# Kernel optimization log

Measured on AMD Instinct MI355X. Metric: run time of the kernel, lower is better.

The kernel has to match this reference:

```python
import jax, jax.numpy as jnp
import numpy as np

B, C, H, W = 4, 128, 64, 64


def setup_inputs() -> dict:
    key = jax.random.key(0)
    ks = jax.random.split(key, 10)
    s = 1.0 / np.sqrt(C)  # conv2d default-ish init scale
    return {
        "key_img": jax.random.normal(ks[0], (B, C, H, W), jnp.float32),
        "query_img": jax.random.normal(ks[1], (B, C, H, W), jnp.float32),
        "value_img": jax.random.normal(ks[2], (B, C, H, W), jnp.float32),
        "Wq": jax.random.normal(ks[3], (C, C), jnp.float32) * s,
        "bq": jax.random.normal(ks[4], (C,), jnp.float32) * s,
        "Wk": jax.random.normal(ks[5], (C, C), jnp.float32) * s,
        "bk": jax.random.normal(ks[6], (C,), jnp.float32) * s,
        "Wv": jax.random.normal(ks[7], (C, C), jnp.float32) * s,
        "bv": jax.random.normal(ks[8], (C,), jnp.float32) * s,
        "gamma": jax.random.normal(ks[9], (1,), jnp.float32) * 0.02,
        "tau": jnp.array([0.01], jnp.float32),  # registered buffer
    }


def _conv1x1(x, Wm, b):
    # 1x1 conv == per-pixel channel mixing
    return jnp.einsum("oc,bchw->bohw", Wm, x) + b[None, :, None, None]


def reference(key_img, query_img, value_img, Wq, bq, Wk, bk, Wv, bv, gamma, tau):
    Bv, Cv, Hv, Wd = key_img.shape
    HW = Hv * Wd
    # proj_query: [B, HW, C], channel-mean-subtracted and L2-normalized per pixel
    pq = _conv1x1(query_img, Wq, bq).reshape(Bv, Cv, HW).transpose(0, 2, 1)
    pq = pq - jnp.mean(pq, axis=2, keepdims=True)
    pq = pq / jnp.linalg.norm(pq, axis=2, keepdims=True)
    # proj_key: [B, C, HW], same normalization along channel axis
    pk = _conv1x1(key_img, Wk, bk).reshape(Bv, Cv, HW)
    pk = pk - jnp.mean(pk, axis=1, keepdims=True)
    pk = pk / jnp.linalg.norm(pk, axis=1, keepdims=True)
    # corr_map: [B, HW, HW] (cosine-similarity-like scores)
    corr_map = jnp.einsum("bnc,bcm->bnm", pq, pk)
    conf_map = jnp.max(corr_map, axis=2).reshape(Bv, 1, Hv, Wd)
    attention = jax.nn.softmax(corr_map / tau[0], axis=-1)
    pv = _conv1x1(value_img, Wv, bv).reshape(Bv, Cv, HW)
    # out = proj_value @ attention^T : [B, C, HW]
    out = jnp.einsum("bcm,bnm->bcn", pv, attention).reshape(Bv, Cv, Hv, Wd)
    out = gamma[0] * out + value_img
    return corr_map, conf_map, out
```

## Files before the change

kernel.cpp:

```cpp
#include <hip/hip_runtime.h>
#include <cstdint>
#include <cstddef>

#define B_   4
#define C_   128
#define HW_  4096

typedef _Float16 h16;
typedef _Float16 h16x8 __attribute__((ext_vector_type(8)));
typedef float f32x4v __attribute__((ext_vector_type(4)));
typedef float f32x16v __attribute__((ext_vector_type(16)));

static __device__ __forceinline__ uint32_t cvtpk(float x, float y) {
  auto h = __builtin_amdgcn_cvt_pkrtz(x, y);
  return __builtin_bit_cast(uint32_t, h);
}

static __device__ __forceinline__ void gload_lds16(const void* g, void* l) {
  __builtin_amdgcn_global_load_lds((const __attribute__((address_space(1))) uint32_t*)g,
                                   (__attribute__((address_space(3))) uint32_t*)l, 16, 0, 0);
}

__global__ __launch_bounds__(256) void proj_kernel(
    const float* __restrict__ qimg, const float* __restrict__ kimg, const float* __restrict__ vimg,
    const float* __restrict__ Wq, const float* __restrict__ bq,
    const float* __restrict__ Wk, const float* __restrict__ bk,
    const float* __restrict__ Wv, const float* __restrict__ bv,
    h16* __restrict__ pq, h16* __restrict__ pk, h16* __restrict__ pv)
{
  __shared__ __align__(16) float sm[9216];
  float* wch = sm;
  float* xs  = sm + 4224;
  float* ps  = sm;

  const int tid   = threadIdx.x;
  const int which = blockIdx.y;
  const int p0g   = blockIdx.x * 64;
  const int b     = p0g >> 12;
  const int p0    = p0g & (HW_ - 1);

  const float* x; const float* W; const float* bias;
  if      (which == 0) { x = qimg; W = Wq; bias = bq; }
  else if (which == 1) { x = kimg; W = Wk; bias = bk; }
  else                 { x = vimg; W = Wv; bias = bv; }
  const float* xb = x + (size_t)b * C_ * HW_ + p0;

  const int ogrp = tid >> 3;
  const int pgrp = tid & 7;
  const int obase = ogrp * 4, pbase = pgrp * 8;

  float acc[4][8];
  #pragma unroll
  for (int i = 0; i < 4; ++i) {
    const float bi = bias[obase + i];
    #pragma unroll
    for (int j = 0; j < 8; ++j) acc[i][j] = bi;
  }

  for (int s = 0; s < 4; ++s) {
    #pragma unroll
    for (int it = 0; it < 16; ++it) {
      const int idx = tid + it * 256;
      const int o = idx >> 5, kc = idx & 31;
      wch[o * 33 + kc] = W[o * 128 + s * 32 + kc];
    }
    #pragma unroll
    for (int it = 0; it < 8; ++it) {
      const int idx = tid + it * 256;
      const int c = idx >> 6, p = idx & 63;
      xs[c * 72 + p] = xb[(size_t)(s * 32 + c) * HW_ + p];
    }
    __syncthreads();
    #pragma unroll 4
    for (int k = 0; k < 32; ++k) {
      const float4 xv0 = *(const float4*)&xs[k * 72 + pbase];
      const float4 xv1 = *(const float4*)&xs[k * 72 + pbase + 4];
      #pragma unroll
      for (int i = 0; i < 4; ++i) {
        const float wv_ = wch[(obase + i) * 33 + k];
        acc[i][0] += wv_ * xv0.x; acc[i][1] += wv_ * xv0.y;
        acc[i][2] += wv_ * xv0.z; acc[i][3] += wv_ * xv0.w;
        acc[i][4] += wv_ * xv1.x; acc[i][5] += wv_ * xv1.y;
        acc[i][6] += wv_ * xv1.z; acc[i][7] += wv_ * xv1.w;
      }
    }
    __syncthreads();
  }

  if (which == 2) {
    h16* dst = pv + (size_t)b * C_ * HW_ + p0;
    #pragma unroll
    for (int i = 0; i < 4; ++i) {
      h16x8 hv;
      #pragma unroll
      for (int j = 0; j < 8; ++j) hv[j] = (h16)acc[i][j];
      *(h16x8*)(dst + (size_t)(obase + i) * HW_ + pbase) = hv;
    }
    return;
  }

  #pragma unroll
  for (int i = 0; i < 4; ++i) {
    float4 v0 = { acc[i][0], acc[i][1], acc[i][2], acc[i][3] };
    float4 v1 = { acc[i][4], acc[i][5], acc[i][6], acc[i][7] };
    *(float4*)&ps[(obase + i) * 72 + pbase]     = v0;
    *(float4*)&ps[(obase + i) * 72 + pbase + 4] = v1;
  }
  __syncthreads();

  const int pr = tid >> 2;
  const int part = tid & 3;
  float sum = 0.f;
  #pragma unroll
  for (int i = 0; i < 32; ++i) sum += ps[(part * 32 + i) * 72 + pr];
  sum += __shfl_xor(sum, 1, 64);
  sum += __shfl_xor(sum, 2, 64);
  const float mean = sum * (1.0f / 128.0f);
  float ssq = 0.f;
  #pragma unroll
  for (int i = 0; i < 32; ++i) {
    const float d = ps[(part * 32 + i) * 72 + pr] - mean;
    ssq += d * d;
  }
  ssq += __shfl_xor(ssq, 1, 64);
  ssq += __shfl_xor(ssq, 2, 64);
  const float inv = 1.0f / sqrtf(ssq);

  h16* dst = (which == 0 ? pq : pk) + (size_t)(p0g + pr) * C_ + part * 32;
  #pragma unroll
  for (int i8 = 0; i8 < 4; ++i8) {
    h16x8 hv;
    #pragma unroll
    for (int j = 0; j < 8; ++j)
      hv[j] = (h16)((ps[(part * 32 + i8 * 8 + j) * 72 + pr] - mean) * inv);
    *(h16x8*)(dst + i8 * 8) = hv;
  }
}

__global__ __launch_bounds__(256, 1) void attn_kernel(
    const h16* __restrict__ pqg, const h16* __restrict__ pkg, const h16* __restrict__ pvg,
    const float* __restrict__ vimg, const float* __restrict__ gp, const float* __restrict__ taup,
    float* __restrict__ corr, float* __restrict__ conf, float* __restrict__ outp)
{
  __shared__ __align__(128) char smem[65536];

  const int tid  = threadIdx.x;
  const int wv   = tid >> 6;
  const int lane = tid & 63;
  const int l31  = lane & 31;
  const int hi   = lane >> 5;
  const int mi   = wv & 1;
  const int nj   = wv >> 1;

  const int bx    = blockIdx.x;
  const int b     = (bx & 7) >> 1;
  const int ntile = ((bx >> 3) << 1) | (bx & 1);
  const int n0    = ntile * 64;

  const float tau   = taup[0];
  const float gamma = gp[0];
  const float kl    = 1.44269504088896340736f / tau;

  h16x8 qf[8];
  {
    const h16* qrow = pqg + ((size_t)(b * HW_ + n0 + nj * 32 + l31)) * C_ + hi * 8;
    #pragma unroll
    for (int kc = 0; kc < 8; ++kc) qf[kc] = *(const h16x8*)(qrow + kc * 16);
  }

  f32x16v oacc[4];
  #pragma unroll
  for (int i = 0; i < 4; ++i) oacc[i] = (f32x16v)0.0f;
  float m_run = -3.0e38f, l_run = 0.0f;

  const char* pkb = (const char*)(pkg + (size_t)b * HW_ * C_);
  const char* pvb = (const char*)(pvg + (size_t)b * C_ * HW_);

  size_t ktoff[4], vtoff[4];
  #pragma unroll
  for (int c4 = 0; c4 < 4; ++c4) {
    const int ch = wv * 4 + c4;
    const int mm = ch * 4 + (lane >> 4);
    const int cb = (lane & 15) * 16;
    ktoff[c4] = (size_t)mm * 256 + (size_t)(cb ^ ((mm & 15) << 4));
    const int cc = ch * 8 + (lane >> 3);
    const int mb = (lane & 7) * 16;
    vtoff[c4] = (size_t)cc * 8192 + (size_t)(mb ^ ((cc & 7) << 4));
  }

  auto STAGE = [&](int tt) {
    const int buf = tt & 1;
    char* ktb = smem + buf * 16384;
    char* vtb = smem + 32768 + buf * 16384;
    const size_t kbase = (size_t)tt * 16384;
    const size_t vbase = (size_t)tt * 128;
    #pragma unroll
    for (int c4 = 0; c4 < 4; ++c4) {
      const int ch = wv * 4 + c4;
      gload_lds16(pkb + kbase + ktoff[c4], ktb + ch * 1024);
    }
    #pragma unroll
    for (int c4 = 0; c4 < 4; ++c4) {
      const int ch = wv * 4 + c4;
      gload_lds16(pvb + vbase + vtoff[c4], vtb + ch * 1024);
    }
  };

  STAGE(0);
  asm volatile("s_waitcnt vmcnt(0)" ::: "memory");
  __builtin_amdgcn_s_barrier();

  for (int t = 0; t < HW_ / 64; ++t) {
    if (t < HW_ / 64 - 1) STAGE(t + 1);

    const int buf = t & 1;
    const char* ktb = smem + buf * 16384;
    const char* vtb = smem + 32768 + buf * 16384;

    f32x16v sacc = (f32x16v)0.0f;
    {
      const int mrow = mi * 32 + l31;
      const char* arow = ktb + mrow * 256;
      const int swz = (mrow & 15) << 4;
      #pragma unroll
      for (int kc = 0; kc < 8; ++kc) {
        const h16x8 af = *(const h16x8*)(arow + ((kc * 32 + hi * 16) ^ swz));
        sacc = __builtin_amdgcn_mfma_f32_32x32x16_f16(af, qf[kc], sacc, 0, 0, 0);
      }
    }

    {
      float* cr = corr + (size_t)(b * HW_ + n0 + nj * 32 + l31) * HW_
                + t * 64 + mi * 32 + hi * 4;
      #pragma unroll
      for (int rq = 0; rq < 4; ++rq) {
        f32x4v v = { sacc[rq * 4 + 0], sacc[rq * 4 + 1], sacc[rq * 4 + 2], sacc[rq * 4 + 3] };
        *(f32x4v*)(cr + rq * 8) = v;
      }
    }

    float tm = sacc[0];
    #pragma unroll
    for (int r = 1; r < 16; ++r) tm = fmaxf(tm, sacc[r]);
    tm = fmaxf(tm, __shfl_xor(tm, 32, 64));
    const float mnew  = fmaxf(m_run, tm);
    const float scale = __builtin_exp2f((m_run - mnew) * kl);
    const float mk    = mnew * kl;
    float ps[16]; float rs = 0.f;
    #pragma unroll
    for (int r = 0; r < 16; ++r) { ps[r] = __builtin_exp2f(sacc[r] * kl - mk); rs += ps[r]; }
    rs += __shfl_xor(rs, 32, 64);
    l_run = l_run * scale + rs;
    m_run = mnew;
    #pragma unroll
    for (int i = 0; i < 4; ++i) oacc[i] *= scale;

    h16x8 pf[2];
    #pragma unroll
    for (int k2 = 0; k2 < 2; ++k2) {
      const int bs = k2 * 8;
      uint32_t a = cvtpk(ps[bs + 0], ps[bs + 1]);
      uint32_t bb = cvtpk(ps[bs + 2], ps[bs + 3]);
      uint32_t c = cvtpk(ps[bs + 4], ps[bs + 5]);
      uint32_t d = cvtpk(ps[bs + 6], ps[bs + 7]);
      asm("v_permlane32_swap_b32 %0, %1" : "+v"(a), "+v"(c));
      asm("v_permlane32_swap_b32 %0, %1" : "+v"(bb), "+v"(d));
      union { uint32_t w[4]; h16x8 h; } u;
      u.w[0] = a; u.w[1] = bb; u.w[2] = c; u.w[3] = d;
      pf[k2] = u.h;
    }

    #pragma unroll
    for (int k2 = 0; k2 < 2; ++k2) {
      #pragma unroll
      for (int cs = 0; cs < 4; ++cs) {
        const int crw = cs * 32 + l31;
        const char* vrow = vtb + crw * 128;
        const int mb = (mi * 64 + k2 * 32 + hi * 16) ^ ((crw & 7) << 4);
        const h16x8 vf = *(const h16x8*)(vrow + mb);
        oacc[cs] = __builtin_amdgcn_mfma_f32_32x32x16_f16(vf, pf[k2], oacc[cs], 0, 0, 0);
      }
    }

    asm volatile("s_waitcnt vmcnt(0)" ::: "memory");
    __builtin_amdgcn_s_barrier();
  }

  float* ms  = (float*)(smem + 32768);
  float* ls  = (float*)(smem + 32768 + 512);
  float* lgi = (float*)(smem + 32768 + 1024);

  if (lane < 32) { ms[wv * 32 + l31] = m_run; ls[wv * 32 + l31] = l_run; }
  __syncthreads();

  const float m0v = ms[nj * 64 + l31], m1v = ms[nj * 64 + 32 + l31];
  const float mg  = fmaxf(m0v, m1v);
  const float lg  = ls[nj * 64 + l31]      * __builtin_exp2f((m0v - mg) * kl)
                  + ls[nj * 64 + 32 + l31] * __builtin_exp2f((m1v - mg) * kl);
  const float fw  = __builtin_exp2f((m_run - mg) * kl);
  if (mi == 0 && lane < 32) {
    lgi[nj * 32 + l31] = 1.0f / lg;
    conf[(size_t)b * HW_ + n0 + nj * 32 + l31] = mg;
  }
  __syncthreads();

  float* otb = (float*)smem;
  #pragma unroll
  for (int p = 0; p < 2; ++p) {
    #pragma unroll
    for (int csl = 0; csl < 2; ++csl) {
      const int cs = p * 2 + csl;
      #pragma unroll
      for (int r = 0; r < 16; ++r) {
        const int cl = ((r & 3) + 8 * (r >> 2) + 4 * hi) + csl * 32;
        otb[((mi * 2 + nj) * 64 + cl) * 32 + l31] = oacc[cs][r] * fw;
      }
    }
    __syncthreads();
    {
      const int n = tid & 31;
      const int rsel = tid >> 5;
      #pragma unroll
      for (int i = 0; i < 16; ++i) {
        const int R = rsel + i * 8;
        const int nj2 = R >> 6, cl = R & 63;
        const int c = p * 64 + cl;
        const float sum = otb[((0 * 2 + nj2) * 64 + cl) * 32 + n]
                        + otb[((1 * 2 + nj2) * 64 + cl) * 32 + n];
        const size_t gi = ((size_t)(b * C_ + c)) * HW_ + n0 + nj2 * 32 + n;
        outp[gi] = gamma * sum * lgi[nj2 * 32 + n] + vimg[gi];
      }
    }
    __syncthreads();
  }
}

extern "C" void kernel_launch(void* const* d_in, const int* in_sizes, int n_in,
                              void* d_out, int out_size, void* d_ws, size_t ws_size,
                              hipStream_t stream) {
  const float* kimg = (const float*)d_in[0];
  const float* qimg = (const float*)d_in[1];
  const float* vimg = (const float*)d_in[2];
  const float* Wq   = (const float*)d_in[3];
  const float* bq   = (const float*)d_in[4];
  const float* Wk   = (const float*)d_in[5];
  const float* bk   = (const float*)d_in[6];
  const float* Wv   = (const float*)d_in[7];
  const float* bv   = (const float*)d_in[8];
  const float* gam  = (const float*)d_in[9];
  const float* tau  = (const float*)d_in[10];

  float* corr = (float*)d_out;
  float* conf = corr + (size_t)B_ * HW_ * HW_;
  float* outp = conf + (size_t)B_ * HW_;

  h16* pq = (h16*)d_ws;
  h16* pk = pq + (size_t)B_ * HW_ * C_;
  h16* pv = pk + (size_t)B_ * HW_ * C_;

  proj_kernel<<<dim3(B_ * HW_ / 64, 3, 1), 256, 0, stream>>>(
      qimg, kimg, vimg, Wq, bq, Wk, bk, Wv, bv, pq, pk, pv);
  attn_kernel<<<dim3(256, 1, 1), 256, 0, stream>>>(
      pq, pk, pv, vimg, gam, tau, corr, conf, outp);
}
```

Baseline: 415.7 us.

## Widen attention block to 8 waves with 128-key tiles and lazy softmax rescale

The attention kernel moves from 256 to 512 threads, with 8 waves splitting each 128-key tile four ways, and staging doubles to 128 KB of LDS. The online-softmax rescale is skipped unless the running max rises past a threshold, and conf is now taken from a separately tracked true max. MFMA sections are wrapped in s_setprio, the wait before the barrier is relaxed to vmcnt(4), and the epilogue reduces four partial accumulators in a single pass. This aims to cut per-tile softmax overhead and improve overlap. In exchange it uses more LDS and registers per block, and the partial wait could race with the async LDS loads.

```diff
diff --git a/kernel.cpp b/kernel.cpp
--- a/kernel.cpp
+++ b/kernel.cpp
@@ -137,20 +137,21 @@
   }
 }
 
-__global__ __launch_bounds__(256, 1) void attn_kernel(
+__global__ __launch_bounds__(512, 2) void attn_kernel(
     const h16* __restrict__ pqg, const h16* __restrict__ pkg, const h16* __restrict__ pvg,
     const float* __restrict__ vimg, const float* __restrict__ gp, const float* __restrict__ taup,
     float* __restrict__ corr, float* __restrict__ conf, float* __restrict__ outp)
 {
-  __shared__ __align__(128) char smem[65536];
+  __shared__ __align__(128) char smem[131072];
+  __shared__ float ms[8 * 32], ls[8 * 32], tms[8 * 32], lgi[2 * 32];
 
   const int tid  = threadIdx.x;
   const int wv   = tid >> 6;
   const int lane = tid & 63;
   const int l31  = lane & 31;
   const int hi   = lane >> 5;
-  const int mi   = wv & 1;
-  const int nj   = wv >> 1;
+  const int mi   = wv & 3;
+  const int nj   = wv >> 2;
 
   const int bx    = blockIdx.x;
   const int b     = (bx & 7) >> 1;
@@ -171,7 +172,7 @@
   f32x16v oacc[4];
   #pragma unroll
   for (int i = 0; i < 4; ++i) oacc[i] = (f32x16v)0.0f;
-  float m_run = -3.0e38f, l_run = 0.0f;
+  float m_run = -3.0e38f, l_run = 0.0f, tmax = -3.0e38f;
 
   const char* pkb = (const char*)(pkg + (size_t)b * HW_ * C_);
   const char* pvb = (const char*)(pvg + (size_t)b * C_ * HW_);
@@ -183,25 +184,21 @@
     const int mm = ch * 4 + (lane >> 4);
     const int cb = (lane & 15) * 16;
     ktoff[c4] = (size_t)mm * 256 + (size_t)(cb ^ ((mm & 15) << 4));
-    const int cc = ch * 8 + (lane >> 3);
-    const int mb = (lane & 7) * 16;
-    vtoff[c4] = (size_t)cc * 8192 + (size_t)(mb ^ ((cc & 7) << 4));
+    const int cc = ch * 4 + (lane >> 4);
+    const int xb2 = (lane & 15) * 16;
+    vtoff[c4] = (size_t)cc * 8192 + (size_t)(xb2 ^ ((cc & 15) << 4));
   }
 
   auto STAGE = [&](int tt) {
     const int buf = tt & 1;
-    char* ktb = smem + buf * 16384;
-    char* vtb = smem + 32768 + buf * 16384;
-    const size_t kbase = (size_t)tt * 16384;
-    const size_t vbase = (size_t)tt * 128;
+    char* ktb = smem + buf * 32768;
+    char* vtb = smem + 65536 + buf * 32768;
+    const size_t kbase = (size_t)tt * 32768;
+    const size_t vbase = (size_t)tt * 256;
     #pragma unroll
     for (int c4 = 0; c4 < 4; ++c4) {
       const int ch = wv * 4 + c4;
       gload_lds16(pkb + kbase + ktoff[c4], ktb + ch * 1024);
-    }
-    #pragma unroll
-    for (int c4 = 0; c4 < 4; ++c4) {
-      const int ch = wv * 4 + c4;
       gload_lds16(pvb + vbase + vtoff[c4], vtb + ch * 1024);
     }
   };
@@ -210,28 +207,30 @@
   asm volatile("s_waitcnt vmcnt(0)" ::: "memory");
   __builtin_amdgcn_s_barrier();
 
-  for (int t = 0; t < HW_ / 64; ++t) {
-    if (t < HW_ / 64 - 1) STAGE(t + 1);
+  for (int t = 0; t < HW_ / 128; ++t) {
+    if (t < HW_ / 128 - 1) STAGE(t + 1);
 
     const int buf = t & 1;
-    const char* ktb = smem + buf * 16384;
-    const char* vtb = smem + 32768 + buf * 16384;
+    const char* ktb = smem + buf * 32768;
+    const char* vtb = smem + 65536 + buf * 32768;
 
     f32x16v sacc = (f32x16v)0.0f;
     {
       const int mrow = mi * 32 + l31;
       const char* arow = ktb + mrow * 256;
       const int swz = (mrow & 15) << 4;
+      __builtin_amdgcn_s_setprio(1);
       #pragma unroll
       for (int kc = 0; kc < 8; ++kc) {
         const h16x8 af = *(const h16x8*)(arow + ((kc * 32 + hi * 16) ^ swz));
         sacc = __builtin_amdgcn_mfma_f32_32x32x16_f16(af, qf[kc], sacc, 0, 0, 0);
       }
+      __builtin_amdgcn_s_setprio(0);
     }
 
     {
       float* cr = corr + (size_t)(b * HW_ + n0 + nj * 32 + l31) * HW_
-                + t * 64 + mi * 32 + hi * 4;
+                + t * 128 + mi * 32 + hi * 4;
       #pragma unroll
       for (int rq = 0; rq < 4; ++rq) {
         f32x4v v = { sacc[rq * 4 + 0], sacc[rq * 4 + 1], sacc[rq * 4 + 2], sacc[rq * 4 + 3] };
@@ -243,17 +242,21 @@
     #pragma unroll
     for (int r = 1; r < 16; ++r) tm = fmaxf(tm, sacc[r]);
     tm = fmaxf(tm, __shfl_xor(tm, 32, 64));
-    const float mnew  = fmaxf(m_run, tm);
-    const float scale = __builtin_exp2f((m_run - mnew) * kl);
-    const float mk    = mnew * kl;
+    tmax = fmaxf(tmax, tm);
+    const float mnew = fmaxf(m_run, tm);
+    if (__any((mnew - m_run) * kl > 8.0f)) {
+      const float scale = __builtin_exp2f((m_run - mnew) * kl);
+      #pragma unroll
+      for (int i = 0; i < 4; ++i) oacc[i] *= scale;
+      l_run *= scale;
+      m_run = mnew;
+    }
+    const float mk = m_run * kl;
     float ps[16]; float rs = 0.f;
     #pragma unroll
     for (int r = 0; r < 16; ++r) { ps[r] = __builtin_exp2f(sacc[r] * kl - mk); rs += ps[r]; }
     rs += __shfl_xor(rs, 32, 64);
-    l_run = l_run * scale + rs;
-    m_run = mnew;
-    #pragma unroll
-    for (int i = 0; i < 4; ++i) oacc[i] *= scale;
+    l_run += rs;
 
     h16x8 pf[2];
     #pragma unroll
@@ -270,68 +273,70 @@
       pf[k2] = u.h;
     }
 
+    __builtin_amdgcn_s_setprio(1);
     #pragma unroll
     for (int k2 = 0; k2 < 2; ++k2) {
       #pragma unroll
       for (int cs = 0; cs < 4; ++cs) {
         const int crw = cs * 32 + l31;
-        const char* vrow = vtb + crw * 128;
-        const int mb = (mi * 64 + k2 * 32 + hi * 16) ^ ((crw & 7) << 4);
+        const char* vrow = vtb + crw * 256;
+        const int mb = (mi * 64 + k2 * 32 + hi * 16) ^ ((crw & 15) << 4);
         const h16x8 vf = *(const h16x8*)(vrow + mb);
         oacc[cs] = __builtin_amdgcn_mfma_f32_32x32x16_f16(vf, pf[k2], oacc[cs], 0, 0, 0);
       }
     }
-
-    asm volatile("s_waitcnt vmcnt(0)" ::: "memory");
+    __builtin_amdgcn_s_setprio(0);
+
+    asm volatile("s_waitcnt vmcnt(4)" ::: "memory");
     __builtin_amdgcn_s_barrier();
   }
 
-  float* ms  = (float*)(smem + 32768);
-  float* ls  = (float*)(smem + 32768 + 512);
-  float* lgi = (float*)(smem + 32768 + 1024);
-
-  if (lane < 32) { ms[wv * 32 + l31] = m_run; ls[wv * 32 + l31] = l_run; }
+  if (lane < 32) {
+    ms[wv * 32 + l31] = m_run; ls[wv * 32 + l31] = l_run; tms[wv * 32 + l31] = tmax;
+  }
   __syncthreads();
 
-  const float m0v = ms[nj * 64 + l31], m1v = ms[nj * 64 + 32 + l31];
-  const float mg  = fmaxf(m0v, m1v);
-  const float lg  = ls[nj * 64 + l31]      * __builtin_exp2f((m0v - mg) * kl)
-                  + ls[nj * 64 + 32 + l31] * __builtin_exp2f((m1v - mg) * kl);
-  const float fw  = __builtin_exp2f((m_run - mg) * kl);
+  float mg = ms[(nj * 4 + 0) * 32 + l31];
+  float tg = tms[(nj * 4 + 0) * 32 + l31];
+  #pragma unroll
+  for (int q = 1; q < 4; ++q) {
+    mg = fmaxf(mg, ms[(nj * 4 + q) * 32 + l31]);
+    tg = fmaxf(tg, tms[(nj * 4 + q) * 32 + l31]);
+  }
+  float lg = 0.f;
+  #pragma unroll
+  for (int q = 0; q < 4; ++q)
+    lg += ls[(nj * 4 + q) * 32 + l31] * __builtin_exp2f((ms[(nj * 4 + q) * 32 + l31] - mg) * kl);
+  const float fw = __builtin_exp2f((m_run - mg) * kl);
   if (mi == 0 && lane < 32) {
     lgi[nj * 32 + l31] = 1.0f / lg;
-    conf[(size_t)b * HW_ + n0 + nj * 32 + l31] = mg;
+    conf[(size_t)b * HW_ + n0 + nj * 32 + l31] = tg;
+  }
+
+  float* otb = (float*)smem;
+  #pragma unroll
+  for (int cs = 0; cs < 4; ++cs) {
+    #pragma unroll
+    for (int r = 0; r < 16; ++r) {
+      const int cl = ((r & 3) + 8 * (r >> 2) + 4 * hi) + cs * 32;
+      otb[((mi * 2 + nj) * 128 + cl) * 32 + l31] = oacc[cs][r] * fw;
+    }
   }
   __syncthreads();
-
-  float* otb = (float*)smem;
-  #pragma unroll
-  for (int p = 0; p < 2; ++p) {
-    #pragma unroll
-    for (int csl = 0; csl < 2; ++csl) {
-      const int cs = p * 2 + csl;
-      #pragma unroll
-      for (int r = 0; r < 16; ++r) {
-        const int cl = ((r & 3) + 8 * (r >> 2) + 4 * hi) + csl * 32;
-        otb[((mi * 2 + nj) * 64 + cl) * 32 + l31] = oacc[cs][r] * fw;
-      }
-    }
-    __syncthreads();
-    {
-      const int n = tid & 31;
-      const int rsel = tid >> 5;
-      #pragma unroll
-      for (int i = 0; i < 16; ++i) {
-        const int R = rsel + i * 8;
-        const int nj2 = R >> 6, cl = R & 63;
-        const int c = p * 64 + cl;
-        const float sum = otb[((0 * 2 + nj2) * 64 + cl) * 32 + n]
-                        + otb[((1 * 2 + nj2) * 64 + cl) * 32 + n];
-        const size_t gi = ((size_t)(b * C_ + c)) * HW_ + n0 + nj2 * 32 + n;
-        outp[gi] = gamma * sum * lgi[nj2 * 32 + n] + vimg[gi];
-      }
-    }
-    __syncthreads();
+  {
+    const int n = tid & 31;
+    const int rsel = tid >> 5;
+    #pragma unroll
+    for (int i = 0; i < 16; ++i) {
+      const int R = rsel + i * 16;
+      const int nj2 = R >> 7, c = R & 127;
+      const float sum = otb[((0 * 2 + nj2) * 128 + c) * 32 + n]
+                      + otb[((1 * 2 + nj2) * 128 + c) * 32 + n]
+                      + otb[((2 * 2 + nj2) * 128 + c) * 32 + n]
+                      + otb[((3 * 2 + nj2) * 128 + c) * 32 + n];
+      const size_t gi = ((size_t)(b * C_ + c)) * HW_ + n0 + nj2 * 32 + n;
+      outp[gi] = gamma * sum * lgi[nj2 * 32 + n] + vimg[gi];
+    }
   }
 }
 
@@ -360,6 +365,6 @@
 
   proj_kernel<<<dim3(B_ * HW_ / 64, 3, 1), 256, 0, stream>>>(
       qimg, kimg, vimg, Wq, bq, Wk, bk, Wv, bv, pq, pk, pv);
-  attn_kernel<<<dim3(256, 1, 1), 256, 0, stream>>>(
+  attn_kernel<<<dim3(256, 1, 1), 512, 0, stream>>>(
       pq, pk, pv, vimg, gam, tau, corr, conf, outp);
 }
```

After: 380.6 us. -8.4%, faster.
